# Performance work log

Hardware: AMD Instinct MI355X
Metric: run time of the kernel (lower is better)

## Reference

```python
import jax, jax.numpy as jnp
import numpy as np


def setup_inputs() -> dict:
    key = jax.random.key(0)
    kq, kk, kv = jax.random.split(key, 3)
    B, H, S, D = 4, 16, 2048, 64
    q = jax.random.normal(kq, (B, H, S, D), dtype=jnp.float32)
    k = jax.random.normal(kk, (B, H, S, D), dtype=jnp.float32)
    v = jax.random.normal(kv, (B, H, S, D), dtype=jnp.float32)
    return {"q": q, "k": k, "v": v}


def reference(q, k, v):
    # SplitScaleAttend (inference, no mask, no dropout):
    # softmax(q k^T / sqrt(d)) v — the chunked loop in the original is a
    # memory-saving schedule of the same math, so one fused expression here.
    scale = q.shape[-1] ** (-0.5)
    # (b h i d),(b h j d) -> (b h i j)
    sim = jnp.einsum("bhid,bhjd->bhij", q, k * scale)
    attn = jax.nn.softmax(sim, axis=-1)
    # (b h i j),(b h j d) -> (b h i d)
    return jnp.einsum("bhij,bhjd->bhid", attn, v)
```

## Files before the change

kernel.cpp:

```cpp
#include <hip/hip_runtime.h>
#include <hip/hip_bf16.h>

typedef __attribute__((ext_vector_type(8))) short short8_t;
typedef __attribute__((ext_vector_type(4))) float f32x4;
typedef __attribute__((ext_vector_type(16))) float f32x16;
typedef __attribute__((ext_vector_type(4))) unsigned u32x4;

static constexpr int B = 4, H = 16, S = 2048, D = 64;
static constexpr int WAVES = 4, QW = 64, QBLK = WAVES * QW;
static constexpr int KVBLK = 64, NT = S / KVBLK;
static constexpr int LDK = 72;

#define QSCALE 0.18033688011112042f

__device__ __forceinline__ unsigned pk2(float a, float b) {
    __hip_bfloat162 h = __float22bfloat162_rn(float2{a, b});
    unsigned u;
    __builtin_memcpy(&u, &h, 4);
    return u;
}

__device__ __forceinline__ float fexp2(float x) {
#if __has_builtin(__builtin_amdgcn_exp2f)
    return __builtin_amdgcn_exp2f(x);
#else
    return exp2f(x);
#endif
}

__device__ __forceinline__ float frcp(float x) {
#if __has_builtin(__builtin_amdgcn_rcpf)
    return __builtin_amdgcn_rcpf(x);
#else
    return 1.f / x;
#endif
}

#define PV2(CD0, CD1, KS)                                                                \
    do {                                                                                 \
        const int h_ = (KS) & 1;                                                         \
        const short8_t vfa =                                                             \
            *reinterpret_cast<const short8_t*>(&Vt[cb][ql][(KS) * 16 + hi * 8]);         \
        const short8_t vfb =                                                             \
            *reinterpret_cast<const short8_t*>(&Vt[cb][32 + ql][(KS) * 16 + hi * 8]);    \
        {                                                                                \
            unsigned x0 = CD0[4 * h_ + 0], y0 = CD0[4 * h_ + 2];                         \
            unsigned x1 = CD0[4 * h_ + 1], y1 = CD0[4 * h_ + 3];                         \
            asm volatile("v_permlane32_swap_b32 %0, %1" : "+v"(x0), "+v"(y0));           \
            asm volatile("v_permlane32_swap_b32 %0, %1" : "+v"(x1), "+v"(y1));           \
            const u32x4 pu = {x0, x1, y0, y1};                                           \
            const short8_t pa = __builtin_bit_cast(short8_t, pu);                        \
            Od00 = __builtin_amdgcn_mfma_f32_32x32x16_bf16(pa, vfa, Od00, 0, 0, 0);      \
            Od01 = __builtin_amdgcn_mfma_f32_32x32x16_bf16(pa, vfb, Od01, 0, 0, 0);      \
            Ol0  = __builtin_amdgcn_mfma_f32_32x32x16_bf16(pa, onesf, Ol0, 0, 0, 0);     \
        }                                                                                \
        {                                                                                \
            unsigned x0 = CD1[4 * h_ + 0], y0 = CD1[4 * h_ + 2];                         \
            unsigned x1 = CD1[4 * h_ + 1], y1 = CD1[4 * h_ + 3];                         \
            asm volatile("v_permlane32_swap_b32 %0, %1" : "+v"(x0), "+v"(y0));           \
            asm volatile("v_permlane32_swap_b32 %0, %1" : "+v"(x1), "+v"(y1));           \
            const u32x4 pu = {x0, x1, y0, y1};                                           \
            const short8_t pa = __builtin_bit_cast(short8_t, pu);                        \
            Od10 = __builtin_amdgcn_mfma_f32_32x32x16_bf16(pa, vfa, Od10, 0, 0, 0);      \
            Od11 = __builtin_amdgcn_mfma_f32_32x32x16_bf16(pa, vfb, Od11, 0, 0, 0);      \
            Ol1  = __builtin_amdgcn_mfma_f32_32x32x16_bf16(pa, onesf, Ol1, 0, 0, 0);     \
        }                                                                                \
    } while (0)

#define QK_HALF(KH, CD0, CD1)                                                            \
    do {                                                                                 \
        f32x16 s0, s1;                                                                   \
        _Pragma("unroll")                                                                \
        for (int r = 0; r < 16; ++r) { s0[r] = 0.f; s1[r] = 0.f; }                       \
        __builtin_amdgcn_s_setprio(1);                                                   \
        _Pragma("unroll")                                                                \
        for (int kc = 0; kc < 4; ++kc) {                                                 \
            const short8_t ka = *reinterpret_cast<const short8_t*>(                      \
                &Ks[cb][(KH) * 32 + ql][kc * 16 + hi * 8]);                              \
            s0 = __builtin_amdgcn_mfma_f32_32x32x16_bf16(ka, qf0[kc], s0, 0, 0, 0);      \
            s1 = __builtin_amdgcn_mfma_f32_32x32x16_bf16(ka, qf1[kc], s1, 0, 0, 0);      \
        }                                                                                \
        __builtin_amdgcn_s_setprio(0);                                                   \
        _Pragma("unroll")                                                                \
        for (int r = 0; r < 16; ++r) s0[r] = fexp2(s0[r]);                               \
        _Pragma("unroll")                                                                \
        for (int r = 0; r < 16; ++r) s1[r] = fexp2(s1[r]);                               \
        _Pragma("unroll")                                                                \
        for (int jj = 0; jj < 8; ++jj) {                                                 \
            CD0[jj] = pk2(s0[jj * 2], s0[jj * 2 + 1]);                                   \
            CD1[jj] = pk2(s1[jj * 2], s1[jj * 2 + 1]);                                   \
        }                                                                                \
    } while (0)

__global__ void __launch_bounds__(256, 2)
attn_fwd(const float* __restrict__ q, const float* __restrict__ k,
         const float* __restrict__ v, float* __restrict__ out) {
    __shared__ short Ks[2][KVBLK][LDK];
    __shared__ short Vt[2][D][LDK];

    const int tid  = threadIdx.x;
    const int lane = tid & 63;
    const int ql   = lane & 31;
    const int hi   = lane >> 5;
    const int wave = tid >> 6;

    const long base = (long)blockIdx.y * S * D;
    const int  q0w  = blockIdx.x * QBLK + wave * QW;

    const u32x4 ones_u = {0x3F803F80u, 0x3F803F80u, 0x3F803F80u, 0x3F803F80u};
    const short8_t onesf = __builtin_bit_cast(short8_t, ones_u);

    short8_t qf0[4], qf1[4];
    #pragma unroll
    for (int qb = 0; qb < 2; ++qb) {
        const float* qp = q + base + (long)(q0w + qb * 32 + ql) * D;
        #pragma unroll
        for (int kc = 0; kc < 4; ++kc) {
            const f32x4 a = *reinterpret_cast<const f32x4*>(qp + kc * 16 + hi * 8);
            const f32x4 b = *reinterpret_cast<const f32x4*>(qp + kc * 16 + hi * 8 + 4);
            const u32x4 u = {pk2(a[0] * QSCALE, a[1] * QSCALE),
                             pk2(a[2] * QSCALE, a[3] * QSCALE),
                             pk2(b[0] * QSCALE, b[1] * QSCALE),
                             pk2(b[2] * QSCALE, b[3] * QSCALE)};
            if (qb == 0) qf0[kc] = __builtin_bit_cast(short8_t, u);
            else         qf1[kc] = __builtin_bit_cast(short8_t, u);
        }
    }

    f32x16 Od00, Od01, Ol0, Od10, Od11, Ol1;
    #pragma unroll
    for (int r = 0; r < 16; ++r) {
        Od00[r] = 0.f; Od01[r] = 0.f; Ol0[r] = 0.f;
        Od10[r] = 0.f; Od11[r] = 0.f; Ol1[r] = 0.f;
    }

    const int kr  = tid >> 2,       kc0 = (tid & 3) * 16;
    const int vk2 = (tid & 31) * 2, vd0 = (tid >> 5) * 8;
    const float* kptr  = k + base + (long)kr * D + kc0;
    const float* vptrA = v + base + (long)vk2 * D + vd0;

    f32x4 kfa = *reinterpret_cast<const f32x4*>(kptr);
    f32x4 kfb = *reinterpret_cast<const f32x4*>(kptr + 4);
    f32x4 kfc = *reinterpret_cast<const f32x4*>(kptr + 8);
    f32x4 kfd = *reinterpret_cast<const f32x4*>(kptr + 12);
    f32x4 vfa0 = *reinterpret_cast<const f32x4*>(vptrA);
    f32x4 vfa1 = *reinterpret_cast<const f32x4*>(vptrA + 4);
    f32x4 vfb0 = *reinterpret_cast<const f32x4*>(vptrA + D);
    f32x4 vfb1 = *reinterpret_cast<const f32x4*>(vptrA + D + 4);

    for (int t = 0; t < NT; ++t) {
        const int cb = t & 1;
        {
            const u32x4 ku0 = {pk2(kfa[0], kfa[1]), pk2(kfa[2], kfa[3]),
                               pk2(kfb[0], kfb[1]), pk2(kfb[2], kfb[3])};
            const u32x4 ku1 = {pk2(kfc[0], kfc[1]), pk2(kfc[2], kfc[3]),
                               pk2(kfd[0], kfd[1]), pk2(kfd[2], kfd[3])};
            *reinterpret_cast<u32x4*>(&Ks[cb][kr][kc0])     = ku0;
            *reinterpret_cast<u32x4*>(&Ks[cb][kr][kc0 + 8]) = ku1;
            #pragma unroll
            for (int j = 0; j < 4; ++j) {
                *reinterpret_cast<unsigned*>(&Vt[cb][vd0 + j][vk2])     = pk2(vfa0[j], vfb0[j]);
                *reinterpret_cast<unsigned*>(&Vt[cb][vd0 + 4 + j][vk2]) = pk2(vfa1[j], vfb1[j]);
            }
        }
        __syncthreads();

        unsigned cd0[8], cd1[8];

        QK_HALF(0, cd0, cd1);

        if (t + 1 < NT) {
            kptr  += KVBLK * D;
            vptrA += KVBLK * D;
            kfa = *reinterpret_cast<const f32x4*>(kptr);
            kfb = *reinterpret_cast<const f32x4*>(kptr + 4);
            kfc = *reinterpret_cast<const f32x4*>(kptr + 8);
            kfd = *reinterpret_cast<const f32x4*>(kptr + 12);
            vfa0 = *reinterpret_cast<const f32x4*>(vptrA);
            vfa1 = *reinterpret_cast<const f32x4*>(vptrA + 4);
            vfb0 = *reinterpret_cast<const f32x4*>(vptrA + D);
            vfb1 = *reinterpret_cast<const f32x4*>(vptrA + D + 4);
        }

        __builtin_amdgcn_s_setprio(1);
        PV2(cd0, cd1, 0);
        PV2(cd0, cd1, 1);
        __builtin_amdgcn_s_setprio(0);

        QK_HALF(1, cd0, cd1);
        __builtin_amdgcn_s_setprio(1);
        PV2(cd0, cd1, 2);
        PV2(cd0, cd1, 3);
        __builtin_amdgcn_s_setprio(0);
    }

    {
        float* op = out + base + (long)q0w * D + ql;
        #pragma unroll
        for (int r = 0; r < 16; ++r) {
            const int   row = (r & 3) + 8 * (r >> 2) + 4 * hi;
            const float s   = frcp(Ol0[r]);
            op[(long)row * D]      = Od00[r] * s;
            op[(long)row * D + 32] = Od01[r] * s;
        }
        float* op1 = op + 32 * D;
        #pragma unroll
        for (int r = 0; r < 16; ++r) {
            const int   row = (r & 3) + 8 * (r >> 2) + 4 * hi;
            const float s   = frcp(Ol1[r]);
            op1[(long)row * D]      = Od10[r] * s;
            op1[(long)row * D + 32] = Od11[r] * s;
        }
    }
}

extern "C" void kernel_launch(void* const* d_in, const int* in_sizes, int n_in,
                              void* d_out, int out_size, void* d_ws, size_t ws_size,
                              hipStream_t stream) {
    const float* q = (const float*)d_in[0];
    const float* k = (const float*)d_in[1];
    const float* v = (const float*)d_in[2];
    float* out = (float*)d_out;
    dim3 grid(S / QBLK, B * H);
    attn_fwd<<<grid, 256, 0, stream>>>(q, k, v, out);
}
```

Before: 101.1 us.

## Compute both QK halves before PV and remap blocks for L2 locality

The inner loop now computes both 32-row halves of the QK scores, exponentiates and packs them, then issues all PV MFMAs together. Previously QK and PV alternated per half. Separately, the 2D grid becomes a 1D grid with a swizzled block-to-(head, q-tile) mapping, so groups of consecutively launched blocks cover 8 heads at once, presumably to shape K/V cache sharing across CUs. The restructured loop keeps twice as many packed score registers live, which raises register pressure under the launch bound of 2 blocks per CU.

Result: faster. 95.83 us (-5.2%).

```diff
diff --git a/kernel.cpp b/kernel.cpp
--- a/kernel.cpp
+++ b/kernel.cpp
@@ -35,6 +35,32 @@
     return 1.f / x;
 #endif
 }
+
+#define QK_MFMA(KH, S0, S1)                                                              \
+    do {                                                                                 \
+        __builtin_amdgcn_s_setprio(1);                                                   \
+        _Pragma("unroll")                                                                \
+        for (int kc = 0; kc < 4; ++kc) {                                                 \
+            const short8_t ka = *reinterpret_cast<const short8_t*>(                      \
+                &Ks[cb][(KH) * 32 + ql][kc * 16 + hi * 8]);                              \
+            S0 = __builtin_amdgcn_mfma_f32_32x32x16_bf16(ka, qf0[kc], S0, 0, 0, 0);      \
+            S1 = __builtin_amdgcn_mfma_f32_32x32x16_bf16(ka, qf1[kc], S1, 0, 0, 0);      \
+        }                                                                                \
+        __builtin_amdgcn_s_setprio(0);                                                   \
+    } while (0)
+
+#define EXP_PACK(S0, S1, CD0, CD1)                                                       \
+    do {                                                                                 \
+        _Pragma("unroll")                                                                \
+        for (int r = 0; r < 16; ++r) S0[r] = fexp2(S0[r]);                               \
+        _Pragma("unroll")                                                                \
+        for (int r = 0; r < 16; ++r) S1[r] = fexp2(S1[r]);                               \
+        _Pragma("unroll")                                                                \
+        for (int jj = 0; jj < 8; ++jj) {                                                 \
+            CD0[jj] = pk2(S0[jj * 2], S0[jj * 2 + 1]);                                   \
+            CD1[jj] = pk2(S1[jj * 2], S1[jj * 2 + 1]);                                   \
+        }                                                                                \
+    } while (0)
 
 #define PV2(CD0, CD1, KS)                                                                \
     do {                                                                                 \
@@ -67,31 +93,6 @@
         }                                                                                \
     } while (0)
 
-#define QK_HALF(KH, CD0, CD1)                                                            \
-    do {                                                                                 \
-        f32x16 s0, s1;                                                                   \
-        _Pragma("unroll")                                                                \
-        for (int r = 0; r < 16; ++r) { s0[r] = 0.f; s1[r] = 0.f; }                       \
-        __builtin_amdgcn_s_setprio(1);                                                   \
-        _Pragma("unroll")                                                                \
-        for (int kc = 0; kc < 4; ++kc) {                                                 \
-            const short8_t ka = *reinterpret_cast<const short8_t*>(                      \
-                &Ks[cb][(KH) * 32 + ql][kc * 16 + hi * 8]);                              \
-            s0 = __builtin_amdgcn_mfma_f32_32x32x16_bf16(ka, qf0[kc], s0, 0, 0, 0);      \
-            s1 = __builtin_amdgcn_mfma_f32_32x32x16_bf16(ka, qf1[kc], s1, 0, 0, 0);      \
-        }                                                                                \
-        __builtin_amdgcn_s_setprio(0);                                                   \
-        _Pragma("unroll")                                                                \
-        for (int r = 0; r < 16; ++r) s0[r] = fexp2(s0[r]);                               \
-        _Pragma("unroll")                                                                \
-        for (int r = 0; r < 16; ++r) s1[r] = fexp2(s1[r]);                               \
-        _Pragma("unroll")                                                                \
-        for (int jj = 0; jj < 8; ++jj) {                                                 \
-            CD0[jj] = pk2(s0[jj * 2], s0[jj * 2 + 1]);                                   \
-            CD1[jj] = pk2(s1[jj * 2], s1[jj * 2 + 1]);                                   \
-        }                                                                                \
-    } while (0)
-
 __global__ void __launch_bounds__(256, 2)
 attn_fwd(const float* __restrict__ q, const float* __restrict__ k,
          const float* __restrict__ v, float* __restrict__ out) {
@@ -104,8 +105,12 @@
     const int hi   = lane >> 5;
     const int wave = tid >> 6;
 
-    const long base = (long)blockIdx.y * S * D;
-    const int  q0w  = blockIdx.x * QBLK + wave * QW;
+    const int lid = blockIdx.x;
+    const int bh  = (lid & 7) | ((lid >> 6) << 3);
+    const int qx  = (lid >> 3) & 7;
+
+    const long base = (long)bh * S * D;
+    const int  q0w  = qx * QBLK + wave * QW;
 
     const u32x4 ones_u = {0x3F803F80u, 0x3F803F80u, 0x3F803F80u, 0x3F803F80u};
     const short8_t onesf = __builtin_bit_cast(short8_t, ones_u);
@@ -165,10 +170,6 @@
         }
         __syncthreads();
 
-        unsigned cd0[8], cd1[8];
-
-        QK_HALF(0, cd0, cd1);
-
         if (t + 1 < NT) {
             kptr  += KVBLK * D;
             vptrA += KVBLK * D;
@@ -182,15 +183,27 @@
             vfb1 = *reinterpret_cast<const f32x4*>(vptrA + D + 4);
         }
 
+        unsigned cdA0[8], cdA1[8], cdB0[8], cdB1[8];
+        {
+            f32x16 s0, s1;
+            #pragma unroll
+            for (int r = 0; r < 16; ++r) { s0[r] = 0.f; s1[r] = 0.f; }
+            QK_MFMA(0, s0, s1);
+            EXP_PACK(s0, s1, cdA0, cdA1);
+        }
+        {
+            f32x16 s0, s1;
+            #pragma unroll
+            for (int r = 0; r < 16; ++r) { s0[r] = 0.f; s1[r] = 0.f; }
+            QK_MFMA(1, s0, s1);
+            EXP_PACK(s0, s1, cdB0, cdB1);
+        }
+
         __builtin_amdgcn_s_setprio(1);
-        PV2(cd0, cd1, 0);
-        PV2(cd0, cd1, 1);
-        __builtin_amdgcn_s_setprio(0);
-
-        QK_HALF(1, cd0, cd1);
-        __builtin_amdgcn_s_setprio(1);
-        PV2(cd0, cd1, 2);
-        PV2(cd0, cd1, 3);
+        PV2(cdA0, cdA1, 0);
+        PV2(cdA0, cdA1, 1);
+        PV2(cdB0, cdB1, 2);
+        PV2(cdB0, cdB1, 3);
         __builtin_amdgcn_s_setprio(0);
     }
 
@@ -221,6 +234,5 @@
     const float* k = (const float*)d_in[1];
     const float* v = (const float*)d_in[2];
     float* out = (float*)d_out;
-    dim3 grid(S / QBLK, B * H);
-    attn_fwd<<<grid, 256, 0, stream>>>(q, k, v, out);
-}
+    attn_fwd<<<dim3((S / QBLK) * B * H), 256, 0, stream>>>(q, k, v, out);
+}
```
